# Optimization experiments

Measured on AMD Instinct MI355X. Metric: run time of the kernel, lower is better.

Reference implementation:

```python
import jax, jax.numpy as jnp
import numpy as np

N = 16384      # nodes (256 chess boards x 64 squares)
E = 393216     # edges (avg degree 24)
G = 256        # graphs
HID = 128
H = 4
C = 32         # head dim
L = 8          # 4 blocks x 2 GATv2Conv
NODE_DIM = 21
EDGE_DIM = 6


def setup_inputs() -> dict:
    key = jax.random.key(0)
    ks = jax.random.split(key, 12)
    x = jax.random.normal(ks[0], (N, NODE_DIM), jnp.float32)
    edge_index = jax.random.randint(ks[1], (2, E), 0, N, dtype=jnp.int32)
    edge_attr = jax.random.uniform(ks[2], (E, EDGE_DIM), dtype=jnp.float32)
    batch = jnp.sort(jax.random.randint(ks[3], (N,), 0, G, dtype=jnp.int32))

    def w(k, shape, fan_in):
        return jax.random.normal(k, shape, jnp.float32) * (1.0 / np.sqrt(fan_in))

    Win = w(ks[4], (NODE_DIM, HID), NODE_DIM)
    b_in = jnp.zeros((HID,), jnp.float32)
    Wl = w(ks[5], (L, HID, HID), HID)
    bl = jnp.zeros((L, HID), jnp.float32)
    Wr = w(ks[6], (L, HID, HID), HID)
    br = jnp.zeros((L, HID), jnp.float32)
    We = w(ks[7], (L, EDGE_DIM, HID), EDGE_DIM)
    att = w(ks[8], (L, H, C), C)
    bconv = jnp.zeros((L, HID), jnp.float32)
    gamma = jnp.ones((L, HID), jnp.float32)
    beta = jnp.zeros((L, HID), jnp.float32)
    W1 = w(ks[9], (HID, 64), HID)
    b1 = jnp.zeros((64,), jnp.float32)
    W2 = w(ks[10], (64, 3), 64)
    b2 = jnp.zeros((3,), jnp.float32)
    return dict(x=x, edge_index=edge_index, edge_attr=edge_attr, batch=batch,
                Win=Win, b_in=b_in, Wl=Wl, bl=bl, Wr=Wr, br=br, We=We, att=att,
                bconv=bconv, gamma=gamma, beta=beta, W1=W1, b1=b1, W2=W2, b2=b2)


def _gatv2(h, src, dst, ea, Wl, bl, Wr, br, We, att, bias):
    # PyG GATv2Conv: message j->i uses x_j from lin_l, x_i from lin_r
    xl = (h @ Wl + bl).reshape(N, H, C)
    xr = (h @ Wr + br).reshape(N, H, C)
    ee = (ea @ We).reshape(-1, H, C)
    m = jax.nn.leaky_relu(xl[src] + xr[dst] + ee, 0.2)   # [Ef, H, C]
    s = jnp.einsum('ehc,hc->eh', m, att)                 # [Ef, H]
    smax = jax.ops.segment_max(s, dst, num_segments=N)   # self-loops => no empty segs
    ex = jnp.exp(s - smax[dst])
    den = jax.ops.segment_sum(ex, dst, num_segments=N)
    alpha = ex / den[dst]                                # edge softmax per target node
    out = jax.ops.segment_sum(alpha[:, :, None] * xl[src], dst, num_segments=N)
    return out.reshape(N, HID) + bias


def _bn(x, g, b):
    mu = jnp.mean(x, axis=0)
    var = jnp.var(x, axis=0)
    return g * (x - mu) * jax.lax.rsqrt(var + 1e-5) + b


def reference(x, edge_index, edge_attr, batch, Win, b_in, Wl, bl, Wr, br, We, att,
              bconv, gamma, beta, W1, b1, W2, b2):
    src0, dst0 = edge_index[0], edge_index[1]
    # add self-loops with fill_value='mean' (per-target mean of incoming edge_attr)
    deg = jax.ops.segment_sum(jnp.ones((E,), jnp.float32), dst0, num_segments=N)
    loop_attr = jax.ops.segment_sum(edge_attr, dst0, num_segments=N) / jnp.maximum(deg, 1.0)[:, None]
    idx = jnp.arange(N, dtype=src0.dtype)
    src = jnp.concatenate([src0, idx])
    dst = jnp.concatenate([dst0, idx])
    ea = jnp.concatenate([edge_attr, loop_attr], axis=0)

    h = jax.nn.relu(x @ Win + b_in)
    for blk in range(4):
        res = h
        l = 2 * blk
        h = jax.nn.relu(_bn(_gatv2(h, src, dst, ea, Wl[l], bl[l], Wr[l], br[l], We[l], att[l], bconv[l]), gamma[l], beta[l]))
        l = 2 * blk + 1
        h = _bn(_gatv2(h, src, dst, ea, Wl[l], bl[l], Wr[l], br[l], We[l], att[l], bconv[l]), gamma[l], beta[l])
        h = jax.nn.relu(h + res)

    cnt = jnp.maximum(jax.ops.segment_sum(jnp.ones((N,), jnp.float32), batch, num_segments=G), 1.0)
    pooled = jax.ops.segment_sum(h, batch, num_segments=G) / cnt[:, None]
    logits = jax.nn.relu(pooled @ W1 + b1) @ W2 + b2
    return logits
```

## Files before the change

kernel.cpp:

```cpp
#include <hip/hip_runtime.h>
#include <hip/hip_fp16.h>
#include <math.h>

constexpr int N   = 16384;
constexpr int E   = 393216;
constexpr int G   = 256;
constexpr int HID = 128;
constexpr int SLOT = 64;

typedef _Float16 f16x8 __attribute__((ext_vector_type(8)));
typedef float    f32x4 __attribute__((ext_vector_type(4)));
typedef float    f32x2 __attribute__((ext_vector_type(2)));

__device__ __forceinline__ float red16(float x) {
    union fi { float f; int i; };
    fi a, b;
    a.f = x;
    b.i = __builtin_amdgcn_mov_dpp(a.i, 0x121, 0xf, 0xf, false); a.f += b.f;
    b.i = __builtin_amdgcn_mov_dpp(a.i, 0x122, 0xf, 0xf, false); a.f += b.f;
    b.i = __builtin_amdgcn_mov_dpp(a.i, 0x124, 0xf, 0xf, false); a.f += b.f;
    b.i = __builtin_amdgcn_mov_dpp(a.i, 0x128, 0xf, 0xf, false); a.f += b.f;
    return a.f;
}

__device__ __forceinline__ f32x2 pk_add(f32x2 a, f32x2 b) {
    f32x2 d;
    asm("v_pk_add_f32 %0, %1, %2" : "=v"(d) : "v"(a), "v"(b));
    return d;
}
__device__ __forceinline__ f32x2 pk_mul(f32x2 a, f32x2 b) {
    f32x2 d;
    asm("v_pk_mul_f32 %0, %1, %2" : "=v"(d) : "v"(a), "v"(b));
    return d;
}
__device__ __forceinline__ f32x2 pk_fma_blo(f32x2 w, f32x2 s, f32x2 c) {
    f32x2 d;
    asm("v_pk_fma_f32 %0, %1, %2, %3 op_sel:[0,0,0] op_sel_hi:[1,0,1]"
        : "=v"(d) : "v"(w), "s"(s), "v"(c));
    return d;
}
__device__ __forceinline__ f32x2 pk_fma_bhi(f32x2 w, f32x2 s, f32x2 c) {
    f32x2 d;
    asm("v_pk_fma_f32 %0, %1, %2, %3 op_sel:[0,1,0] op_sel_hi:[1,1,1]"
        : "=v"(d) : "v"(w), "s"(s), "v"(c));
    return d;
}

__global__ __launch_bounds__(256) void k_scatter(const int* __restrict__ src,
                                                 const int* __restrict__ dst,
                                                 int* __restrict__ fill,
                                                 const float* __restrict__ edge_attr,
                                                 int* __restrict__ csr_src,
                                                 float* __restrict__ csr_ea) {
    int e = blockIdx.x * 256 + threadIdx.x;
    if (e >= E) return;
    int d = dst[e];
    int pos = atomicAdd(&fill[d], 1);
    if (pos > 62) return;
    size_t base = (size_t)d * SLOT + pos;
    csr_src[base] = src[e];
    const float* s = edge_attr + (size_t)e * 6;
    float4 a = {s[0], s[1], s[2], s[3]};
    float4 b = {s[4], s[5], 0.0f, 0.0f};
    float4* dstp = (float4*)(csr_ea + base * 8);
    dstp[0] = a;
    dstp[1] = b;
}

__global__ __launch_bounds__(256) void k_loopattr2(const int* __restrict__ fill,
                                                   int* __restrict__ csr_src,
                                                   float* __restrict__ csr_ea) {
    int i = blockIdx.x * 256 + threadIdx.x;
    if (i >= N) return;
    int deg = fill[i];
    deg = deg > 62 ? 62 : deg;
    size_t e0 = (size_t)i * SLOT;
    float4 sa = {0, 0, 0, 0};
    float sbx = 0.0f, sby = 0.0f;
    for (int e = 0; e < deg; e++) {
        const float4* p = (const float4*)(csr_ea + (e0 + e) * 8);
        float4 a = p[0];
        float4 b = p[1];
        sa.x += a.x; sa.y += a.y; sa.z += a.z; sa.w += a.w;
        sbx += b.x; sby += b.y;
    }
    float inv = 1.0f / fmaxf((float)deg, 1.0f);
    float4 oa = {sa.x * inv, sa.y * inv, sa.z * inv, sa.w * inv};
    float4 ob = {sbx * inv, sby * inv, 0.0f, 0.0f};
    float4* q = (float4*)(csr_ea + (e0 + deg) * 8);
    q[0] = oa;
    q[1] = ob;
    csr_src[e0 + deg] = i;
}

__global__ __launch_bounds__(128) void k_ingemm(const float* __restrict__ x,
                                                const float* __restrict__ Win,
                                                const float* __restrict__ b_in,
                                                float* __restrict__ h) {
    __shared__ float xs[21];
    int i = blockIdx.x;
    int c = threadIdx.x;
    if (c < 21) xs[c] = x[i * 21 + c];
    __syncthreads();
    float acc = b_in[c];
#pragma unroll
    for (int d = 0; d < 21; d++) acc += xs[d] * Win[d * HID + c];
    h[i * HID + c] = fmaxf(acc, 0.0f);
}

__global__ __launch_bounds__(128) void k_prepw(const float* __restrict__ Wl,
                                               const float* __restrict__ Wr,
                                               _Float16* __restrict__ WT) {
    int b = blockIdx.x;
    int col = b & 127;
    int mat = (b >> 7) & 1;
    int l = b >> 8;
    int k = threadIdx.x;
    const float* W = mat ? Wr : Wl;
    float w = W[((size_t)l * 128 + k) * 128 + col];
    _Float16 hi = (_Float16)w;
    _Float16 lo = (_Float16)(w - (float)hi);
    size_t base = ((size_t)(l * 2 + mat) * 2) << 14;
    WT[base + (size_t)col * 128 + k] = hi;
    WT[base + 16384 + (size_t)col * 128 + k] = lo;
}

#define BN4(V, S, H) { V.x = fmaf(V.x, S.x, H.x); V.y = fmaf(V.y, S.y, H.y); \
                       V.z = fmaf(V.z, S.z, H.z); V.w = fmaf(V.w, S.w, H.w); }
#define ADD4(V, R)   { float4 _r = (R); V.x += _r.x; V.y += _r.y; \
                       V.z += _r.z; V.w += _r.w; }
#define RELU4(V)     { V.x = fmaxf(V.x, 0.f); V.y = fmaxf(V.y, 0.f); \
                       V.z = fmaxf(V.z, 0.f); V.w = fmaxf(V.w, 0.f); }
#define SPLIT(F, HIV, LOV, IDX) { float _f = (F); _Float16 _h = (_Float16)_f; \
                       HIV[IDX] = _h; LOV[IDX] = (_Float16)(_f - (float)_h); }

__global__ __launch_bounds__(256) void k_gemm_lr(const float* __restrict__ h,
                                                 const float* __restrict__ bns,
                                                 const float* __restrict__ gamma,
                                                 const float* __restrict__ beta,
                                                 float* __restrict__ res,
                                                 const _Float16* __restrict__ WT,
                                                 const float* __restrict__ bl,
                                                 const float* __restrict__ br,
                                                 __half* __restrict__ XLh,
                                                 float* __restrict__ XR) {
    __shared__ _Float16 hs_hi[32][136];
    __shared__ _Float16 hs_lo[32][136];
    __shared__ float sc[HID], sh[HID];
    int t = threadIdx.x;
    int r0 = blockIdx.x * 32;
    if (bns) {
        if (t < 128) {
            const float invN = 1.0f / (float)N;
            float mean = bns[t] * invN;
            float var  = bns[128 + t] * invN - mean * mean;
            float inv  = rsqrtf(var + 1e-5f);
            float s = gamma[t] * inv;
            sc[t] = s;
            sh[t] = beta[t] - mean * s;
        }
        __syncthreads();
    }
    {
        int row = t >> 3;
        int cb  = (t & 7) * 16;
        size_t base = (size_t)(r0 + row) * HID + cb;
        const float4* srcp = (const float4*)&h[base];
        float4 v0 = srcp[0], v1 = srcp[1], v2 = srcp[2], v3 = srcp[3];
        if (bns) {
            float4 s0 = *(const float4*)&sc[cb];
            float4 s1 = *(const float4*)&sc[cb + 4];
            float4 s2 = *(const float4*)&sc[cb + 8];
            float4 s3 = *(const float4*)&sc[cb + 12];
            float4 h0 = *(const float4*)&sh[cb];
            float4 h1 = *(const float4*)&sh[cb + 4];
            float4 h2 = *(const float4*)&sh[cb + 8];
            float4 h3 = *(const float4*)&sh[cb + 12];
            BN4(v0, s0, h0); BN4(v1, s1, h1); BN4(v2, s2, h2); BN4(v3, s3, h3);
            if (res) {
                const float4* rp = (const float4*)&res[base];
                ADD4(v0, rp[0]); ADD4(v1, rp[1]); ADD4(v2, rp[2]); ADD4(v3, rp[3]);
            }
            RELU4(v0); RELU4(v1); RELU4(v2); RELU4(v3);
            if (res) {
                float4* wp = (float4*)&res[base];
                wp[0] = v0; wp[1] = v1; wp[2] = v2; wp[3] = v3;
            }
        }
        f16x8 hi0, hi1, lo0, lo1;
        SPLIT(v0.x, hi0, lo0, 0) SPLIT(v0.y, hi0, lo0, 1)
        SPLIT(v0.z, hi0, lo0, 2) SPLIT(v0.w, hi0, lo0, 3)
        SPLIT(v1.x, hi0, lo0, 4) SPLIT(v1.y, hi0, lo0, 5)
        SPLIT(v1.z, hi0, lo0, 6) SPLIT(v1.w, hi0, lo0, 7)
        SPLIT(v2.x, hi1, lo1, 0) SPLIT(v2.y, hi1, lo1, 1)
        SPLIT(v2.z, hi1, lo1, 2) SPLIT(v2.w, hi1, lo1, 3)
        SPLIT(v3.x, hi1, lo1, 4) SPLIT(v3.y, hi1, lo1, 5)
        SPLIT(v3.z, hi1, lo1, 6) SPLIT(v3.w, hi1, lo1, 7)
        *(f16x8*)&hs_hi[row][cb]     = hi0;
        *(f16x8*)&hs_hi[row][cb + 8] = hi1;
        *(f16x8*)&hs_lo[row][cb]     = lo0;
        *(f16x8*)&hs_lo[row][cb + 8] = lo1;
    }
    __syncthreads();

    int wv   = t >> 6;
    int lane = t & 63;
    int mat  = wv >> 1;
    int ch   = wv & 1;
    int ln15 = lane & 15;
    int kg   = lane >> 4;
    const _Float16* Whi = WT + ((size_t)mat * 2) * 16384;
    const float* bias = mat ? br : bl;
    f32x4 acc[2][4];
#pragma unroll
    for (int c = 0; c < 4; c++) {
        float bv = bias[(ch * 4 + c) * 16 + ln15];
        f32x4 b4 = {bv, bv, bv, bv};
        acc[0][c] = b4;
        acc[1][c] = b4;
    }
#pragma unroll
    for (int kt = 0; kt < 4; kt++) {
        int k0 = kt * 32 + kg * 8;
        f16x8 ahi0 = *(const f16x8*)&hs_hi[ln15][k0];
        f16x8 ahi1 = *(const f16x8*)&hs_hi[16 + ln15][k0];
        f16x8 alo0 = *(const f16x8*)&hs_lo[ln15][k0];
        f16x8 alo1 = *(const f16x8*)&hs_lo[16 + ln15][k0];
#pragma unroll
        for (int c = 0; c < 4; c++) {
            int col = (ch * 4 + c) * 16 + ln15;
            const _Float16* wp = Whi + (size_t)col * 128 + k0;
            f16x8 bhi = *(const f16x8*)wp;
            f16x8 blo = *(const f16x8*)(wp + 16384);
            acc[0][c] = __builtin_amdgcn_mfma_f32_16x16x32_f16(ahi0, bhi, acc[0][c], 0, 0, 0);
            acc[1][c] = __builtin_amdgcn_mfma_f32_16x16x32_f16(ahi1, bhi, acc[1][c], 0, 0, 0);
            acc[0][c] = __builtin_amdgcn_mfma_f32_16x16x32_f16(alo0, bhi, acc[0][c], 0, 0, 0);
            acc[1][c] = __builtin_amdgcn_mfma_f32_16x16x32_f16(alo1, bhi, acc[1][c], 0, 0, 0);
            acc[0][c] = __builtin_amdgcn_mfma_f32_16x16x32_f16(ahi0, blo, acc[0][c], 0, 0, 0);
            acc[1][c] = __builtin_amdgcn_mfma_f32_16x16x32_f16(ahi1, blo, acc[1][c], 0, 0, 0);
        }
    }
#pragma unroll
    for (int rt = 0; rt < 2; rt++) {
        int rowb = r0 + rt * 16 + kg * 4;
#pragma unroll
        for (int c = 0; c < 4; c++) {
            int col = (ch * 4 + c) * 16 + ln15;
            if (mat) {
#pragma unroll
                for (int r = 0; r < 4; r++)
                    XR[(size_t)(rowb + r) * 128 + col] = acc[rt][c][r];
            } else {
#pragma unroll
                for (int r = 0; r < 4; r++)
                    XLh[(size_t)(rowb + r) * 128 + col] = __float2half(acc[rt][c][r]);
            }
        }
    }
}

__global__ __launch_bounds__(256, 4) void k_edge(const int* __restrict__ fill,
                                                 const int* __restrict__ csr_src,
                                                 const float* __restrict__ csr_ea,
                                                 const __half2* __restrict__ xlh,
                                                 const float* __restrict__ xr,
                                                 const float* __restrict__ We_l,
                                                 const float* __restrict__ att_l,
                                                 float* __restrict__ gout) {
    int iv = (blockIdx.x * 256 + threadIdx.x) >> 6;
    int i = __builtin_amdgcn_readfirstlane(iv);
    int lane = threadIdx.x & 63;
    int hh = lane >> 4;
    int ss = lane & 15;
    int ch0 = hh * 32 + 2 * ss;

    const float LOG2E = 1.44269504088896f;
    float a0 = att_l[ch0] * LOG2E, a1 = att_l[ch0 + 1] * LOG2E;
    f32x2 wep[6];
#pragma unroll
    for (int d = 0; d < 6; d++) {
        float2 wv = *(const float2*)&We_l[d * HID + ch0];
        wep[d] = (f32x2){wv.x, wv.y};
    }
    const f32x2 c02 = {0.2f, 0.2f};

    float2 xr2 = *(const float2*)&xr[(size_t)i * HID + ch0];
    f32x2 xr2v = {xr2.x, xr2.y};
    float rd = 0.0f, acc0 = 0.0f, acc1 = 0.0f;
    int deg = __builtin_amdgcn_readfirstlane(fill[i]);
    deg = deg > 62 ? 62 : deg;
    int e0 = i * SLOT;
    int e1 = e0 + deg + 1;
    int nedge = deg + 1;
    int nfull = nedge >> 2;
    int efull = e0 + (nfull << 2);

    auto ld_idx = [&](int e, int out[4]) {
#pragma unroll
        for (int k = 0; k < 4; k++) {
            int ec = e + k;
            ec = (ec < e1) ? ec : (e1 - 1);
            out[k] = __builtin_amdgcn_readfirstlane(csr_src[ec]);
        }
    };
    auto ld_xl = [&](const int idx[4], __half2 out[4]) {
#pragma unroll
        for (int k = 0; k < 4; k++)
            out[k] = xlh[(size_t)idx[k] * 64 + lane];
    };
    auto ld_ea = [&](int e, f32x2 oA[4], f32x2 oB[4], f32x2 oC[4]) {
#pragma unroll
        for (int k = 0; k < 4; k++) {
            const float* p = csr_ea + (size_t)(e + k) * 8;
            oA[k] = *(const f32x2*)p;
            oB[k] = *(const f32x2*)(p + 2);
            oC[k] = *(const f32x2*)(p + 4);
        }
    };
    auto edge1 = [&](__half2 xlv, f32x2 eA, f32x2 eB, f32x2 eC) -> float {
        float2 xf = __half22float2(xlv);
        f32x2 xf2 = {xf.x, xf.y};
        f32x2 m = pk_add(xf2, xr2v);
        m = pk_fma_blo(wep[0], eA, m);
        m = pk_fma_bhi(wep[1], eA, m);
        m = pk_fma_blo(wep[2], eB, m);
        m = pk_fma_bhi(wep[3], eB, m);
        m = pk_fma_blo(wep[4], eC, m);
        m = pk_fma_bhi(wep[5], eC, m);
        f32x2 tl = pk_mul(m, c02);
        float m0 = fmaxf(m[0], tl[0]);
        float m1 = fmaxf(m[1], tl[1]);
        float pv = m0 * a0;
        pv = fmaf(m1, a1, pv);
        return red16(pv);
    };
    auto bodyF = [&](const __half2 xlv[4], const f32x2 eA[4],
                     const f32x2 eB[4], const f32x2 eC[4]) {
#pragma unroll
        for (int k = 0; k < 4; k++) {
            float pv = edge1(xlv[k], eA[k], eB[k], eC[k]);
            float ex = exp2f(pv);
            rd += ex;
            float2 xf = __half22float2(xlv[k]);
            acc0 = fmaf(ex, xf.x, acc0);
            acc1 = fmaf(ex, xf.y, acc1);
        }
    };

    int iA[4], iB[4];
    __half2 x0[4], x1[4];
    f32x2 A0[4], B0[4], C0[4], A1[4], B1[4], C1[4];
    ld_idx(e0, iA);
    ld_idx(e0 + 4, iB);
    ld_xl(iA, x0);
    ld_ea(e0, A0, B0, C0);
    int e = e0, nf = nfull;
    while (nf >= 2) {
        ld_idx(e + 8, iA);
        ld_xl(iB, x1);
        ld_ea(e + 4, A1, B1, C1);
        bodyF(x0, A0, B0, C0);
        ld_idx(e + 12, iB);
        ld_xl(iA, x0);
        ld_ea(e + 8, A0, B0, C0);
        bodyF(x1, A1, B1, C1);
        e += 8; nf -= 2;
    }
    if (nf == 1) {
        bodyF(x0, A0, B0, C0);
    }
    int rem = nedge & 3;
    if (rem) {
        int it[4];
        __half2 xt[4];
        ld_idx(efull, it);
        ld_xl(it, xt);
#pragma unroll
        for (int k = 0; k < 4; k++) {
            int ee = efull + k;
            int ec = (ee < e1) ? ee : (e1 - 1);
            const float* p = csr_ea + (size_t)ec * 8;
            f32x2 eA = *(const f32x2*)p;
            f32x2 eB = *(const f32x2*)(p + 2);
            f32x2 eC = *(const f32x2*)(p + 4);
            float pv = edge1(xt[k], eA, eB, eC);
            pv = (ee < e1) ? pv : -INFINITY;
            float ex = exp2f(pv);
            rd += ex;
            float2 xf = __half22float2(xt[k]);
            acc0 = fmaf(ex, xf.x, acc0);
            acc1 = fmaf(ex, xf.y, acc1);
        }
    }
    float inv = 1.0f / rd;
    float2 o = {acc0 * inv, acc1 * inv};
    *(float2*)&gout[(size_t)i * HID + ch0] = o;
}

__global__ __launch_bounds__(256) void k_bnstats(const float* __restrict__ v,
                                                 float* __restrict__ sums) {
    __shared__ float l_s[256], l_q[256];
    int t = threadIdx.x;
    int c = t & 127;
    int half = t >> 7;
    int r = blockIdx.x * 64 + half;
    float s = 0.0f, q = 0.0f;
    for (int it = 0; it < 32; it++, r += 2) {
        float val = v[(size_t)r * HID + c];
        s += val;
        q = fmaf(val, val, q);
    }
    l_s[t] = s; l_q[t] = q;
    __syncthreads();
    if (t < 128) {
        s = l_s[t] + l_s[t + 128];
        atomicAdd(&sums[c], s);
    } else {
        q = l_q[t] + l_q[t - 128];
        atomicAdd(&sums[128 + c], q);
    }
}

__global__ __launch_bounds__(128) void k_pool(const float* __restrict__ gout,
                                              const float* __restrict__ res,
                                              const float* __restrict__ bns,
                                              const float* __restrict__ gamma,
                                              const float* __restrict__ beta,
                                              const int* __restrict__ batch,
                                              const float* __restrict__ W1,
                                              const float* __restrict__ b1,
                                              const float* __restrict__ W2,
                                              const float* __restrict__ b2,
                                              float* __restrict__ out) {
    __shared__ float pooled[HID];
    __shared__ float hid[64];
    __shared__ int bounds[2];
    int g = blockIdx.x;
    int t = threadIdx.x;
    if (t < 2) {
        int target = g + t;
        int lo = 0, hi = N;
        while (lo < hi) {
            int mid = (lo + hi) >> 1;
            if (batch[mid] < target) lo = mid + 1; else hi = mid;
        }
        bounds[t] = lo;
    }
    const float invN = 1.0f / (float)N;
    float mean = bns[t] * invN;
    float var  = bns[128 + t] * invN - mean * mean;
    float scb  = gamma[t] * rsqrtf(var + 1e-5f);
    float shb  = beta[t] - mean * scb;
    __syncthreads();
    int s = bounds[0], e = bounds[1];
    float acc = 0.0f;
    for (int r = s; r < e; r++) {
        float v = fmaf(gout[(size_t)r * HID + t], scb, shb) + res[(size_t)r * HID + t];
        acc += fmaxf(v, 0.0f);
    }
    float cntf = fmaxf((float)(e - s), 1.0f);
    pooled[t] = acc / cntf;
    __syncthreads();
    if (t < 64) {
        float a = b1[t];
#pragma unroll 4
        for (int c = 0; c < HID; c++) a += pooled[c] * W1[c * 64 + t];
        hid[t] = fmaxf(a, 0.0f);
    }
    __syncthreads();
    if (t < 3) {
        float a = b2[t];
#pragma unroll
        for (int j = 0; j < 64; j++) a += hid[j] * W2[j * 3 + t];
        out[g * 3 + t] = a;
    }
}

extern "C" void kernel_launch(void* const* d_in, const int* in_sizes, int n_in,
                              void* d_out, int out_size, void* d_ws, size_t ws_size,
                              hipStream_t stream) {
    const float* x         = (const float*)d_in[0];
    const int*   edge_index= (const int*)d_in[1];
    const float* edge_attr = (const float*)d_in[2];
    const int*   batch     = (const int*)d_in[3];
    const float* Win       = (const float*)d_in[4];
    const float* b_in      = (const float*)d_in[5];
    const float* Wl        = (const float*)d_in[6];
    const float* bl        = (const float*)d_in[7];
    const float* Wr        = (const float*)d_in[8];
    const float* br        = (const float*)d_in[9];
    const float* We        = (const float*)d_in[10];
    const float* att       = (const float*)d_in[11];
    const float* gamma     = (const float*)d_in[13];
    const float* beta      = (const float*)d_in[14];
    const float* W1        = (const float*)d_in[15];
    const float* b1        = (const float*)d_in[16];
    const float* W2        = (const float*)d_in[17];
    const float* b2        = (const float*)d_in[18];
    float* out = (float*)d_out;

    const int* src0 = edge_index;
    const int* dst0 = edge_index + E;

    char* ws = (char*)d_ws;
    size_t off = 0;
    auto alloc = [&](size_t bytes) -> void* {
        void* p = ws + off;
        off += (bytes + 255) & ~(size_t)255;
        return p;
    };
    int*      fill      = (int*)alloc((size_t)N * sizeof(int));
    float*    bnsums    = (float*)alloc((size_t)8 * 256 * sizeof(float));
    int*      csr_src   = (int*)alloc((size_t)N * SLOT * sizeof(int));
    float*    csr_ea    = (float*)alloc((size_t)N * SLOT * 8 * sizeof(float) + 512);
    float*    H0        = (float*)alloc((size_t)N * HID * sizeof(float));
    __half*   XLh       = (__half*)alloc((size_t)N * HID * sizeof(__half));
    float*    XR        = (float*)alloc((size_t)N * HID * sizeof(float));
    float*    GOUT      = (float*)alloc((size_t)N * HID * sizeof(float));
    _Float16* WT        = (_Float16*)alloc((size_t)8 * 4 * 16384 * 2);

    size_t zbytes = (size_t)N * sizeof(int) + 8 * 256 * sizeof(float);
    hipMemsetAsync(fill, 0, zbytes, stream);
    k_scatter<<<(E + 255) / 256, 256, 0, stream>>>(src0, dst0, fill,
                                                   edge_attr, csr_src, csr_ea);
    k_loopattr2<<<(N + 255) / 256, 256, 0, stream>>>(fill, csr_src, csr_ea);
    k_prepw<<<8 * 2 * 128, 128, 0, stream>>>(Wl, Wr, WT);
    k_ingemm<<<N, 128, 0, stream>>>(x, Win, b_in, H0);

    for (int l = 0; l < 8; l++) {
        bool odd = (l & 1) != 0;
        const float* hin;
        const float* bns_in = nullptr;
        const float* g_in = nullptr;
        const float* b_in2 = nullptr;
        float* res = nullptr;
        if (l == 0) {
            hin = H0;
        } else {
            hin = GOUT;
            bns_in = bnsums + (l - 1) * 256;
            g_in  = gamma + (size_t)(l - 1) * HID;
            b_in2 = beta  + (size_t)(l - 1) * HID;
            if (!odd) res = H0;
        }
        k_gemm_lr<<<N / 32, 256, 0, stream>>>(hin, bns_in, g_in, b_in2, res,
                                              WT + (size_t)l * 4 * 16384,
                                              bl + l * HID, br + l * HID,
                                              XLh, XR);
        k_edge<<<N / 4, 256, 0, stream>>>(fill, csr_src, csr_ea,
                                          (const __half2*)XLh, XR,
                                          We + (size_t)l * 6 * HID,
                                          att + (size_t)l * HID, GOUT);
        k_bnstats<<<256, 256, 0, stream>>>(GOUT, bnsums + l * 256);
    }
    k_pool<<<G, 128, 0, stream>>>(GOUT, H0, bnsums + 7 * 256,
                                  gamma + 7 * HID, beta + 7 * HID,
                                  batch, W1, b1, W2, b2, out);
}
```

Measured before the change: 659.1 us.

## Vectorize bnstats loads, split edge FMA chain, use float2 edge_attr reads

Three unrelated tweaks. The BN statistics kernel now reads float4 per thread with an unrolled loop and a tree reduction in shared memory, replacing scalar strided loads. The per-edge attention computation splits a serial chain of six packed FMAs into two shorter chains to expose more instruction-level parallelism. The scatter kernel reads edge attributes as three float2 loads instead of six scalars. Together these cut load instruction count and dependency latency, at the cost of an extra packed add and more synchronizations in the stats kernel.

After: 817.3 us. 24.0% more time.

```diff
diff --git a/kernel.cpp b/kernel.cpp
--- a/kernel.cpp
+++ b/kernel.cpp
@@ -31,6 +31,12 @@
 __device__ __forceinline__ f32x2 pk_mul(f32x2 a, f32x2 b) {
     f32x2 d;
     asm("v_pk_mul_f32 %0, %1, %2" : "=v"(d) : "v"(a), "v"(b));
+    return d;
+}
+__device__ __forceinline__ f32x2 pk_mul_bhi(f32x2 w, f32x2 s) {
+    f32x2 d;
+    asm("v_pk_mul_f32 %0, %1, %2 op_sel:[0,1] op_sel_hi:[1,1]"
+        : "=v"(d) : "v"(w), "s"(s));
     return d;
 }
 __device__ __forceinline__ f32x2 pk_fma_blo(f32x2 w, f32x2 s, f32x2 c) {
@@ -59,9 +65,10 @@
     if (pos > 62) return;
     size_t base = (size_t)d * SLOT + pos;
     csr_src[base] = src[e];
-    const float* s = edge_attr + (size_t)e * 6;
-    float4 a = {s[0], s[1], s[2], s[3]};
-    float4 b = {s[4], s[5], 0.0f, 0.0f};
+    const float2* s2 = (const float2*)(edge_attr + (size_t)e * 6);
+    float2 p0 = s2[0], p1 = s2[1], p2 = s2[2];
+    float4 a = {p0.x, p0.y, p1.x, p1.y};
+    float4 b = {p2.x, p2.y, 0.0f, 0.0f};
     float4* dstp = (float4*)(csr_ea + base * 8);
     dstp[0] = a;
     dstp[1] = b;
@@ -324,9 +331,10 @@
         m = pk_fma_blo(wep[0], eA, m);
         m = pk_fma_bhi(wep[1], eA, m);
         m = pk_fma_blo(wep[2], eB, m);
-        m = pk_fma_bhi(wep[3], eB, m);
-        m = pk_fma_blo(wep[4], eC, m);
-        m = pk_fma_bhi(wep[5], eC, m);
+        f32x2 tc = pk_mul_bhi(wep[3], eB);
+        tc = pk_fma_blo(wep[4], eC, tc);
+        tc = pk_fma_bhi(wep[5], eC, tc);
+        m = pk_add(m, tc);
         f32x2 tl = pk_mul(m, c02);
         float m0 = fmaxf(m[0], tl[0]);
         float m1 = fmaxf(m[1], tl[1]);
@@ -399,25 +407,49 @@
 
 __global__ __launch_bounds__(256) void k_bnstats(const float* __restrict__ v,
                                                  float* __restrict__ sums) {
-    __shared__ float l_s[256], l_q[256];
+    __shared__ float4 l_s[256], l_q[256];
     int t = threadIdx.x;
-    int c = t & 127;
-    int half = t >> 7;
-    int r = blockIdx.x * 64 + half;
-    float s = 0.0f, q = 0.0f;
-    for (int it = 0; it < 32; it++, r += 2) {
-        float val = v[(size_t)r * HID + c];
-        s += val;
-        q = fmaf(val, val, q);
+    int cq = (t & 31) * 4;
+    int r  = blockIdx.x * 64 + (t >> 5);
+    float4 s = {0, 0, 0, 0}, q = {0, 0, 0, 0};
+#pragma unroll
+    for (int it = 0; it < 8; it++, r += 8) {
+        float4 val = *(const float4*)&v[(size_t)r * HID + cq];
+        s.x += val.x; s.y += val.y; s.z += val.z; s.w += val.w;
+        q.x = fmaf(val.x, val.x, q.x); q.y = fmaf(val.y, val.y, q.y);
+        q.z = fmaf(val.z, val.z, q.z); q.w = fmaf(val.w, val.w, q.w);
     }
     l_s[t] = s; l_q[t] = q;
     __syncthreads();
     if (t < 128) {
-        s = l_s[t] + l_s[t + 128];
-        atomicAdd(&sums[c], s);
-    } else {
-        q = l_q[t] + l_q[t - 128];
-        atomicAdd(&sums[128 + c], q);
+        float4 a = l_s[t], b = l_s[t + 128];
+        a.x += b.x; a.y += b.y; a.z += b.z; a.w += b.w; l_s[t] = a;
+        float4 c = l_q[t], d = l_q[t + 128];
+        c.x += d.x; c.y += d.y; c.z += d.z; c.w += d.w; l_q[t] = c;
+    }
+    __syncthreads();
+    if (t < 64) {
+        float4 a = l_s[t], b = l_s[t + 64];
+        a.x += b.x; a.y += b.y; a.z += b.z; a.w += b.w; l_s[t] = a;
+        float4 c = l_q[t], d = l_q[t + 64];
+        c.x += d.x; c.y += d.y; c.z += d.z; c.w += d.w; l_q[t] = c;
+    }
+    __syncthreads();
+    if (t < 32) {
+        float4 a = l_s[t], b = l_s[t + 32];
+        a.x += b.x; a.y += b.y; a.z += b.z; a.w += b.w;
+        atomicAdd(&sums[cq],     a.x);
+        atomicAdd(&sums[cq + 1], a.y);
+        atomicAdd(&sums[cq + 2], a.z);
+        atomicAdd(&sums[cq + 3], a.w);
+    } else if (t < 64) {
+        int cq2 = ((t - 32) & 31) * 4;
+        float4 c = l_q[t - 32], d = l_q[t];
+        c.x += d.x; c.y += d.y; c.z += d.z; c.w += d.w;
+        atomicAdd(&sums[128 + cq2],     c.x);
+        atomicAdd(&sums[128 + cq2 + 1], c.y);
+        atomicAdd(&sums[128 + cq2 + 2], c.z);
+        atomicAdd(&sums[128 + cq2 + 3], c.w);
     }
 }
 
```
